# Kernel tuning notes

Measured on AMD Instinct MI355X. Metric: run time of the kernel, lower is better.

Reference implementation:

```python
import jax, jax.numpy as jnp
import numpy as np

N_USERS = 50000
N_ITEMS = 50000
N_NODES = N_USERS + N_ITEMS
N_EDGES = 1600000
D_IN = 128
D_OUT = 128


def setup_inputs() -> dict:
    key = jax.random.key(0)
    k1, k2, k3, k4, k5, k6 = jax.random.split(key, 6)
    u_f = jax.random.normal(k1, (N_USERS, D_IN), dtype=jnp.float32)
    v_f = jax.random.normal(k2, (N_ITEMS, D_IN), dtype=jnp.float32)
    adj_rows = jax.random.randint(k3, (N_EDGES,), 0, N_NODES, dtype=jnp.int32)
    adj_cols = jax.random.randint(k4, (N_EDGES,), 0, N_NODES, dtype=jnp.int32)
    adj_vals = jax.random.uniform(k5, (N_EDGES,), dtype=jnp.float32)
    # xavier_uniform init for weight [in_feats, out_feats]
    bound = float(np.sqrt(6.0 / (D_IN + D_OUT)))
    weight = jax.random.uniform(k6, (D_IN, D_OUT), dtype=jnp.float32,
                                minval=-bound, maxval=bound)
    return {"u_f": u_f, "v_f": v_f, "adj_rows": adj_rows,
            "adj_cols": adj_cols, "adj_vals": adj_vals, "weight": weight}


def reference(u_f, v_f, adj_rows, adj_cols, adj_vals, weight):
    # node_f = cat([u_f, v_f]) @ W          -- dense transform
    node_f = jnp.concatenate([u_f, v_f], axis=0)          # [N, D_in]
    node_f = node_f @ weight                               # [N, D_out]
    # sparse adjacency matmul: out[r] = sum_e vals[e] * node_f[cols[e]]
    msgs = adj_vals[:, None] * node_f[adj_cols]            # [E, D_out]
    out = jax.ops.segment_sum(msgs, adj_rows, num_segments=N_NODES)
    # activation (relu)
    return jax.nn.relu(out)
```

## Files before the change

kernel.cpp:

```cpp
#include <hip/hip_runtime.h>
#include <hip/hip_bf16.h>
#include <hip/hip_fp16.h>

#define N_USERS 50000
#define N_NODES 100000
#define N_EDGES 1600000
#define DIM 128
#define CAP 64
#define GEMM_BLOCKS 512
#define FILL_BLOCKS (N_EDGES / 256)

typedef __attribute__((ext_vector_type(8))) _Float16 half8;
typedef __attribute__((ext_vector_type(4))) float f32x4;

__global__ void zero_counts_kernel(int* __restrict__ counts) {
    int i = blockIdx.x * blockDim.x + threadIdx.x;
    if (i < N_NODES) counts[i] = 0;
}

__device__ __forceinline__ void gemm_body(
        const float* __restrict__ u_f, const float* __restrict__ v_f,
        const float* __restrict__ W, _Float16* __restrict__ node_f,
        _Float16* wfrag, int blockId, int nBlocks) {
    const int tid = threadIdx.x;

    for (int f = tid * 64, end = tid * 64 + 64; f < end; ++f) {
        const int ts   = f >> 9;
        const int rem  = f & 511;
        const int ln   = rem >> 3;
        const int j    = rem & 7;
        const int t    = ts >> 2;
        const int s    = ts & 3;
        const int krow = s * 32 + (ln >> 4) * 8 + j;
        const int col  = t * 16 + (ln & 15);
        wfrag[f] = (_Float16)W[krow * DIM + col];
    }
    __syncthreads();

    const int lane = tid & 63;
    const int wave = tid >> 6;
    const int m    = lane & 15;
    const int quad = lane >> 4;
    const int n_wtiles = N_NODES / 16;

    for (int wt = blockId * 4 + wave; wt < n_wtiles; wt += nBlocks * 4) {
        const int row = wt * 16 + m;
        const float* src = (row < N_USERS) ? u_f + (size_t)row * DIM
                                           : v_f + (size_t)(row - N_USERS) * DIM;
        f32x4 acc[8];
        #pragma unroll
        for (int t = 0; t < 8; ++t) acc[t] = (f32x4){0.f, 0.f, 0.f, 0.f};

        #pragma unroll
        for (int s = 0; s < 4; ++s) {
            const float* ap = src + s * 32 + quad * 8;
            const float4 a0 = *(const float4*)ap;
            const float4 a1 = *(const float4*)(ap + 4);
            half8 af;
            af[0] = (_Float16)a0.x; af[1] = (_Float16)a0.y;
            af[2] = (_Float16)a0.z; af[3] = (_Float16)a0.w;
            af[4] = (_Float16)a1.x; af[5] = (_Float16)a1.y;
            af[6] = (_Float16)a1.z; af[7] = (_Float16)a1.w;
            #pragma unroll
            for (int t = 0; t < 8; ++t) {
                const half8 wf = *(const half8*)&wfrag[((t * 4 + s) * 64 + lane) * 8];
                acc[t] = __builtin_amdgcn_mfma_f32_16x16x32_f16(af, wf, acc[t], 0, 0, 0);
            }
        }

        const int base = wt * 16;
        #pragma unroll
        for (int t = 0; t < 8; ++t) {
            #pragma unroll
            for (int r = 0; r < 4; ++r) {
                const int orow = base + quad * 4 + r;
                node_f[(size_t)orow * DIM + t * 16 + m] = (_Float16)acc[t][r];
            }
        }
    }
}

__global__ __launch_bounds__(256) void fused_gemm_fill_kernel(
        const float* __restrict__ u_f, const float* __restrict__ v_f,
        const float* __restrict__ W, _Float16* __restrict__ node_f,
        const int* __restrict__ rows, const int* __restrict__ cols,
        const float* __restrict__ vals,
        int* __restrict__ counts, int2* __restrict__ buckets) {
    __shared__ _Float16 wfrag[32 * 64 * 8];
    if (blockIdx.x < GEMM_BLOCKS) {
        gemm_body(u_f, v_f, W, node_f, wfrag, blockIdx.x, GEMM_BLOCKS);
    } else {
        const int e = (blockIdx.x - GEMM_BLOCKS) * 256 + threadIdx.x;
        const int r = rows[e];
        const int slot = atomicAdd(&counts[r], 1);
        if (slot < CAP) {
            int2 p;
            p.x = cols[e];
            p.y = __float_as_int(vals[e]);
            buckets[(size_t)r * CAP + slot] = p;
        }
    }
}

__global__ __launch_bounds__(256) void gemm_mfma_kernel(
        const float* __restrict__ u_f, const float* __restrict__ v_f,
        const float* __restrict__ W, _Float16* __restrict__ node_f) {
    __shared__ _Float16 wfrag[32 * 64 * 8];
    gemm_body(u_f, v_f, W, node_f, wfrag, blockIdx.x, gridDim.x);
}

__global__ __launch_bounds__(256) void gather_kernel(
        const _Float16* __restrict__ node_f, const int* __restrict__ counts,
        const int2* __restrict__ buckets, float* __restrict__ out) {
    const int row  = (blockIdx.x * blockDim.x + threadIdx.x) >> 6;
    const int lane = threadIdx.x & 63;
    if (row >= N_NODES) return;

    int cnt = counts[row];
    if (cnt > CAP) cnt = CAP;

    int   col = 0;
    float val = 0.f;
    if (lane < cnt) {
        const int2 p = buckets[(size_t)row * CAP + lane];
        col = p.x;
        val = __int_as_float(p.y);
    }

    const size_t lofs = (size_t)(lane * 2);
    float2 acc = {0.f, 0.f};
    int j = 0;
    for (; j + 4 <= cnt; j += 4) {
        const int c0 = __shfl(col, j,     64);
        const int c1 = __shfl(col, j + 1, 64);
        const int c2 = __shfl(col, j + 2, 64);
        const int c3 = __shfl(col, j + 3, 64);
        const float v0 = __shfl(val, j,     64);
        const float v1 = __shfl(val, j + 1, 64);
        const float v2 = __shfl(val, j + 2, 64);
        const float v3 = __shfl(val, j + 3, 64);
        const __half2 h0 = *(const __half2*)&node_f[(size_t)c0 * DIM + lofs];
        const __half2 h1 = *(const __half2*)&node_f[(size_t)c1 * DIM + lofs];
        const __half2 h2 = *(const __half2*)&node_f[(size_t)c2 * DIM + lofs];
        const __half2 h3 = *(const __half2*)&node_f[(size_t)c3 * DIM + lofs];
        const float2 f0 = __half22float2(h0);
        const float2 f1 = __half22float2(h1);
        const float2 f2 = __half22float2(h2);
        const float2 f3 = __half22float2(h3);
        acc.x += v0 * f0.x; acc.y += v0 * f0.y;
        acc.x += v1 * f1.x; acc.y += v1 * f1.y;
        acc.x += v2 * f2.x; acc.y += v2 * f2.y;
        acc.x += v3 * f3.x; acc.y += v3 * f3.y;
    }
    for (; j < cnt; ++j) {
        const int   c = __shfl(col, j, 64);
        const float v = __shfl(val, j, 64);
        const __half2 h = *(const __half2*)&node_f[(size_t)c * DIM + lofs];
        const float2 nf = __half22float2(h);
        acc.x += v * nf.x;
        acc.y += v * nf.y;
    }
    float2 r2;
    r2.x = acc.x > 0.f ? acc.x : 0.f;
    r2.y = acc.y > 0.f ? acc.y : 0.f;
    *(float2*)&out[(size_t)row * DIM + lofs] = r2;
}

__global__ void zero_out_kernel(float* __restrict__ out) {
    int i = blockIdx.x * blockDim.x + threadIdx.x;
    int idx = i * 4;
    if (idx < N_NODES * DIM) {
        float4 z = {0.f, 0.f, 0.f, 0.f};
        *(float4*)&out[idx] = z;
    }
}

__global__ void scatter_kernel(const _Float16* __restrict__ node_f,
                               const int* __restrict__ rows, const int* __restrict__ cols,
                               const float* __restrict__ vals, float* __restrict__ out) {
    int t = blockIdx.x * blockDim.x + threadIdx.x;
    int e = t >> 5;
    int part = t & 31;
    if (e >= N_EDGES) return;
    int r = rows[e], c = cols[e];
    float v = vals[e];
    const __half2 h0 = *(const __half2*)&node_f[(size_t)c * DIM + part * 4];
    const __half2 h1 = *(const __half2*)&node_f[(size_t)c * DIM + part * 4 + 2];
    const float2 f0 = __half22float2(h0);
    const float2 f1 = __half22float2(h1);
    float* dst = &out[(size_t)r * DIM + part * 4];
    unsafeAtomicAdd(dst + 0, v * f0.x);
    unsafeAtomicAdd(dst + 1, v * f0.y);
    unsafeAtomicAdd(dst + 2, v * f1.x);
    unsafeAtomicAdd(dst + 3, v * f1.y);
}

__global__ void relu_kernel(float* __restrict__ out) {
    int i = blockIdx.x * blockDim.x + threadIdx.x;
    int idx = i * 4;
    if (idx < N_NODES * DIM) {
        float4 v = *(float4*)&out[idx];
        v.x = v.x > 0.f ? v.x : 0.f;
        v.y = v.y > 0.f ? v.y : 0.f;
        v.z = v.z > 0.f ? v.z : 0.f;
        v.w = v.w > 0.f ? v.w : 0.f;
        *(float4*)&out[idx] = v;
    }
}

extern "C" void kernel_launch(void* const* d_in, const int* in_sizes, int n_in,
                              void* d_out, int out_size, void* d_ws, size_t ws_size,
                              hipStream_t stream) {
    const float* u_f  = (const float*)d_in[0];
    const float* v_f  = (const float*)d_in[1];
    const int*   rows = (const int*)d_in[2];
    const int*   cols = (const int*)d_in[3];
    const float* vals = (const float*)d_in[4];
    const float* W    = (const float*)d_in[5];
    float* out = (float*)d_out;

    char* ws = (char*)d_ws;
    const size_t nodef_bytes  = (size_t)N_NODES * DIM * 2;
    const size_t counts_bytes = (size_t)N_NODES * 4;
    const size_t bucket_bytes = (size_t)N_NODES * CAP * 8;

    _Float16* node_f = (_Float16*)ws;
    int*  counts  = (int*)(ws + nodef_bytes);
    int2* buckets = (int2*)(ws + nodef_bytes + counts_bytes);

    if (ws_size >= nodef_bytes + counts_bytes + bucket_bytes) {
        zero_counts_kernel<<<(N_NODES + 255) / 256, 256, 0, stream>>>(counts);
        fused_gemm_fill_kernel<<<GEMM_BLOCKS + FILL_BLOCKS, 256, 0, stream>>>(
            u_f, v_f, W, node_f, rows, cols, vals, counts, buckets);
        gather_kernel<<<(N_NODES * 64 + 255) / 256, 256, 0, stream>>>(
            node_f, counts, buckets, out);
    } else {
        gemm_mfma_kernel<<<512, 256, 0, stream>>>(u_f, v_f, W, node_f);
        zero_out_kernel<<<(N_NODES * DIM / 4 + 255) / 256, 256, 0, stream>>>(out);
        scatter_kernel<<<((size_t)N_EDGES * 32 + 255) / 256, 256, 0, stream>>>(
            node_f, rows, cols, vals, out);
        relu_kernel<<<(N_NODES * DIM / 4 + 255) / 256, 256, 0, stream>>>(out);
    }
}
```

Before: 268.5 us.

## Interleave GEMM and bucket-fill blocks, widen gather loads to half4 split-wave

```diff
diff --git a/kernel.cpp b/kernel.cpp
--- a/kernel.cpp
+++ b/kernel.cpp
@@ -7,15 +7,18 @@
 #define N_EDGES 1600000
 #define DIM 128
 #define CAP 64
+
 #define GEMM_BLOCKS 512
-#define FILL_BLOCKS (N_EDGES / 256)
+#define FILL_BLOCKS ((N_EDGES + 1023) / 1024)
+#define FUSED_GRID (2048 + (FILL_BLOCKS - 1536))
 
 typedef __attribute__((ext_vector_type(8))) _Float16 half8;
+typedef __attribute__((ext_vector_type(4))) _Float16 half4;
 typedef __attribute__((ext_vector_type(4))) float f32x4;
 
 __global__ void zero_counts_kernel(int* __restrict__ counts) {
     int i = blockIdx.x * blockDim.x + threadIdx.x;
-    if (i < N_NODES) counts[i] = 0;
+    if (i < N_NODES / 4) ((int4*)counts)[i] = (int4){0, 0, 0, 0};
 }
 
 __device__ __forceinline__ void gemm_body(
@@ -85,19 +88,28 @@
         const float* __restrict__ W, _Float16* __restrict__ node_f,
         const int* __restrict__ rows, const int* __restrict__ cols,
         const float* __restrict__ vals,
-        int* __restrict__ counts, int2* __restrict__ buckets) {
+        int* __restrict__ counts, long long* __restrict__ buckets) {
     __shared__ _Float16 wfrag[32 * 64 * 8];
-    if (blockIdx.x < GEMM_BLOCKS) {
-        gemm_body(u_f, v_f, W, node_f, wfrag, blockIdx.x, GEMM_BLOCKS);
-    } else {
-        const int e = (blockIdx.x - GEMM_BLOCKS) * 256 + threadIdx.x;
-        const int r = rows[e];
-        const int slot = atomicAdd(&counts[r], 1);
-        if (slot < CAP) {
-            int2 p;
-            p.x = cols[e];
-            p.y = __float_as_int(vals[e]);
-            buckets[(size_t)r * CAP + slot] = p;
+    const int b = blockIdx.x;
+    const int q = b >> 2, rbit = b & 3;
+
+    if (b < 2048 && rbit == 0) {
+        gemm_body(u_f, v_f, W, node_f, wfrag, q, GEMM_BLOCKS);
+        return;
+    }
+    const int fid = (b < 2048) ? (q * 3 + rbit - 1) : (1536 + b - 2048);
+    const int ebase = fid * 1024 + threadIdx.x;
+    #pragma unroll
+    for (int k = 0; k < 4; ++k) {
+        const int e = ebase + k * 256;
+        if (e < N_EDGES) {
+            const int r = rows[e];
+            const int slot = atomicAdd(&counts[r], 1);
+            if (slot < CAP) {
+                const long long packed =
+                    ((long long)__float_as_int(vals[e]) << 32) | (unsigned)cols[e];
+                __builtin_nontemporal_store(packed, &buckets[(size_t)r * CAP + slot]);
+            }
         }
     }
 }
@@ -111,10 +123,12 @@
 
 __global__ __launch_bounds__(256) void gather_kernel(
         const _Float16* __restrict__ node_f, const int* __restrict__ counts,
-        const int2* __restrict__ buckets, float* __restrict__ out) {
+        const long long* __restrict__ buckets, float* __restrict__ out) {
     const int row  = (blockIdx.x * blockDim.x + threadIdx.x) >> 6;
     const int lane = threadIdx.x & 63;
     if (row >= N_NODES) return;
+    const int pid = lane >> 5;
+    const int cl  = lane & 31;
 
     int cnt = counts[row];
     if (cnt > CAP) cnt = CAP;
@@ -122,48 +136,63 @@
     int   col = 0;
     float val = 0.f;
     if (lane < cnt) {
-        const int2 p = buckets[(size_t)row * CAP + lane];
-        col = p.x;
-        val = __int_as_float(p.y);
-    }
-
-    const size_t lofs = (size_t)(lane * 2);
-    float2 acc = {0.f, 0.f};
+        const long long p =
+            __builtin_nontemporal_load(&buckets[(size_t)row * CAP + lane]);
+        col = (int)(unsigned)p;
+        val = __int_as_float((int)(p >> 32));
+    }
+
+    f32x4 acc = {0.f, 0.f, 0.f, 0.f};
     int j = 0;
-    for (; j + 4 <= cnt; j += 4) {
-        const int c0 = __shfl(col, j,     64);
-        const int c1 = __shfl(col, j + 1, 64);
-        const int c2 = __shfl(col, j + 2, 64);
-        const int c3 = __shfl(col, j + 3, 64);
-        const float v0 = __shfl(val, j,     64);
-        const float v1 = __shfl(val, j + 1, 64);
-        const float v2 = __shfl(val, j + 2, 64);
-        const float v3 = __shfl(val, j + 3, 64);
-        const __half2 h0 = *(const __half2*)&node_f[(size_t)c0 * DIM + lofs];
-        const __half2 h1 = *(const __half2*)&node_f[(size_t)c1 * DIM + lofs];
-        const __half2 h2 = *(const __half2*)&node_f[(size_t)c2 * DIM + lofs];
-        const __half2 h3 = *(const __half2*)&node_f[(size_t)c3 * DIM + lofs];
-        const float2 f0 = __half22float2(h0);
-        const float2 f1 = __half22float2(h1);
-        const float2 f2 = __half22float2(h2);
-        const float2 f3 = __half22float2(h3);
-        acc.x += v0 * f0.x; acc.y += v0 * f0.y;
-        acc.x += v1 * f1.x; acc.y += v1 * f1.y;
-        acc.x += v2 * f2.x; acc.y += v2 * f2.y;
-        acc.x += v3 * f3.x; acc.y += v3 * f3.y;
-    }
-    for (; j < cnt; ++j) {
+    for (; j + 8 <= cnt; j += 8) {
+        int c[4]; float v[4]; half4 h[4];
+        #pragma unroll
+        for (int p = 0; p < 4; ++p) {
+            c[p] = __shfl(col, j + 2 * p + pid, 64);
+            v[p] = __shfl(val, j + 2 * p + pid, 64);
+        }
+        #pragma unroll
+        for (int p = 0; p < 4; ++p)
+            h[p] = *(const half4*)&node_f[(size_t)c[p] * DIM + cl * 4];
+        #pragma unroll
+        for (int p = 0; p < 4; ++p) {
+            acc[0] += v[p] * (float)h[p][0];
+            acc[1] += v[p] * (float)h[p][1];
+            acc[2] += v[p] * (float)h[p][2];
+            acc[3] += v[p] * (float)h[p][3];
+        }
+    }
+    for (; j + 2 <= cnt; j += 2) {
+        const int   c = __shfl(col, j + pid, 64);
+        const float v = __shfl(val, j + pid, 64);
+        const half4 h = *(const half4*)&node_f[(size_t)c * DIM + cl * 4];
+        acc[0] += v * (float)h[0];
+        acc[1] += v * (float)h[1];
+        acc[2] += v * (float)h[2];
+        acc[3] += v * (float)h[3];
+    }
+    if (j < cnt) {
         const int   c = __shfl(col, j, 64);
-        const float v = __shfl(val, j, 64);
-        const __half2 h = *(const __half2*)&node_f[(size_t)c * DIM + lofs];
-        const float2 nf = __half22float2(h);
-        acc.x += v * nf.x;
-        acc.y += v * nf.y;
-    }
-    float2 r2;
-    r2.x = acc.x > 0.f ? acc.x : 0.f;
-    r2.y = acc.y > 0.f ? acc.y : 0.f;
-    *(float2*)&out[(size_t)row * DIM + lofs] = r2;
+        const float vv = __shfl(val, j, 64);
+        const float v = pid ? 0.f : vv;
+        const half4 h = *(const half4*)&node_f[(size_t)c * DIM + cl * 4];
+        acc[0] += v * (float)h[0];
+        acc[1] += v * (float)h[1];
+        acc[2] += v * (float)h[2];
+        acc[3] += v * (float)h[3];
+    }
+
+    #pragma unroll
+    for (int i = 0; i < 4; ++i) acc[i] += __shfl_xor(acc[i], 32, 64);
+
+    if (pid == 0) {
+        f32x4 r;
+        r[0] = acc[0] > 0.f ? acc[0] : 0.f;
+        r[1] = acc[1] > 0.f ? acc[1] : 0.f;
+        r[2] = acc[2] > 0.f ? acc[2] : 0.f;
+        r[3] = acc[3] > 0.f ? acc[3] : 0.f;
+        __builtin_nontemporal_store(r, (f32x4*)&out[(size_t)row * DIM + cl * 4]);
+    }
 }
 
 __global__ void zero_out_kernel(float* __restrict__ out) {
@@ -225,12 +254,12 @@
     const size_t bucket_bytes = (size_t)N_NODES * CAP * 8;
 
     _Float16* node_f = (_Float16*)ws;
-    int*  counts  = (int*)(ws + nodef_bytes);
-    int2* buckets = (int2*)(ws + nodef_bytes + counts_bytes);
+    int* counts = (int*)(ws + nodef_bytes);
+    long long* buckets = (long long*)(ws + nodef_bytes + counts_bytes);
 
     if (ws_size >= nodef_bytes + counts_bytes + bucket_bytes) {
-        zero_counts_kernel<<<(N_NODES + 255) / 256, 256, 0, stream>>>(counts);
-        fused_gemm_fill_kernel<<<GEMM_BLOCKS + FILL_BLOCKS, 256, 0, stream>>>(
+        zero_counts_kernel<<<(N_NODES / 4 + 255) / 256, 256, 0, stream>>>(counts);
+        fused_gemm_fill_kernel<<<FUSED_GRID, 256, 0, stream>>>(
             u_f, v_f, W, node_f, rows, cols, vals, counts, buckets);
         gather_kernel<<<(N_NODES * 64 + 255) / 256, 256, 0, stream>>>(
             node_f, counts, buckets, out);
```

Result: slower. 301.0 us (+12.1%).
